# Kernel tuning notes

Hardware: AMD Instinct MI355X
Metric: run time of the kernel (lower is better)

Reference implementation:

```python
import jax, jax.numpy as jnp
import numpy as np


def setup_inputs() -> dict:
    key = jax.random.key(0)
    ks = jax.random.split(key, 6)
    B, S, D, G, I, H = 4, 2048, 1024, 256, 1024, 16
    return {
        "inputs_embeds": jax.random.normal(ks[0], (B, S, D), dtype=jnp.float32),
        "structure_features": jax.random.normal(ks[1], (B, G), dtype=jnp.float32),
        "Wq": jax.random.normal(ks[2], (D, I), dtype=jnp.float32) * 0.02,
        "Wk": jax.random.normal(ks[3], (G, I), dtype=jnp.float32) * 0.02,
        "Wv": jax.random.normal(ks[4], (D, I), dtype=jnp.float32) * 0.02,
        "Wo": jax.random.normal(ks[5], (I, D), dtype=jnp.float32) * 0.02,
        "num_heads": 16,
    }


def reference(inputs_embeds, structure_features, Wq, Wk, Wv, Wo, num_heads):
    B, S, D = inputs_embeds.shape
    I = Wq.shape[1]
    H = num_heads
    hd = I // H
    scale = 1.0 / (hd ** 0.5)

    # queries/values from token embeddings: [B, S, I] -> [B, H, S, hd]
    q = (inputs_embeds @ Wq).reshape(B, S, H, hd).transpose(0, 2, 1, 3)
    v = (inputs_embeds @ Wv).reshape(B, S, H, hd).transpose(0, 2, 1, 3)

    # structure_features is repeat-expanded to seq_len in the original; the
    # projection of identical rows is identical, so project once and broadcast.
    k1 = (structure_features @ Wk).reshape(B, 1, H, hd).transpose(0, 2, 1, 3)  # [B, H, 1, hd]
    k = jnp.broadcast_to(k1, (B, H, S, hd))  # same values as key_proj(repeated sf)

    # [B, H, S, S] score matrix (columns identical by construction, as in the
    # original module) -> softmax -> weighted sum of values.
    scores = jnp.einsum("bhqd,bhkd->bhqk", q, k) * scale
    probs = jax.nn.softmax(scores, axis=-1)
    attended = jnp.einsum("bhqk,bhkd->bhqd", probs, v)  # [B, H, S, hd]

    attended = attended.transpose(0, 2, 1, 3).reshape(B, S, I)
    return attended @ Wo
```

## Files before the change

### kernel.cpp

```cpp
#include <hip/hip_runtime.h>

#define BB 4
#define SS 2048
#define DD 1024
#define II 1024


constexpr int JP = 128;
constexpr int ROWS1 = SS / JP;

typedef float f4 __attribute__((ext_vector_type(4)));

__global__ __launch_bounds__(256)
void k1_partial(const float4* __restrict__ x, float4* __restrict__ pbuf) {
    const int g = blockIdx.x;
    const float4* xr = x + (size_t)g * ROWS1 * (DD / 4) + threadIdx.x;
    float4 a = make_float4(0.f, 0.f, 0.f, 0.f);
    #pragma unroll
    for (int r = 0; r < ROWS1; ++r) {
        float4 v = xr[(size_t)r * (DD / 4)];
        a.x += v.x; a.y += v.y; a.z += v.z; a.w += v.w;
    }
    pbuf[(size_t)g * (DD / 4) + threadIdx.x] = a;
}

__global__ __launch_bounds__(256)
void kred(const float4* __restrict__ pbuf, float4* __restrict__ xbar) {
    const int b = blockIdx.x >> 4, dg = blockIdx.x & 15;
    const int c4 = threadIdx.x & 15;
    const int jg = threadIdx.x >> 4;
    const float4* p = pbuf + ((size_t)b * JP + jg * 8) * (DD / 4) + dg * 16 + c4;
    float4 a = make_float4(0.f, 0.f, 0.f, 0.f);
    #pragma unroll
    for (int j = 0; j < 8; ++j) {
        float4 v = p[(size_t)j * (DD / 4)];
        a.x += v.x; a.y += v.y; a.z += v.z; a.w += v.w;
    }
    __shared__ float4 red[16][16];
    red[jg][c4] = a;
    __syncthreads();
    if (threadIdx.x < 16) {
        float4 s = make_float4(0.f, 0.f, 0.f, 0.f);
        #pragma unroll
        for (int q = 0; q < 16; ++q) {
            float4 v = red[q][threadIdx.x];
            s.x += v.x; s.y += v.y; s.z += v.z; s.w += v.w;
        }
        const float sc = 1.0f / (float)SS;
        xbar[b * (DD / 4) + dg * 16 + threadIdx.x] =
            make_float4(s.x * sc, s.y * sc, s.z * sc, s.w * sc);
    }
}

__global__ __launch_bounds__(1024)
void kg_gemv_b(const float4* __restrict__ vec, const float* __restrict__ W,
               float* __restrict__ out) {
    __shared__ float xs[DD];
    const int cg = blockIdx.x & 63;
    const int b  = blockIdx.x >> 6;
    const int tid = threadIdx.x;
    if (tid < DD / 4) ((f4*)xs)[tid] = ((const f4*)vec)[b * (DD / 4) + tid];
    __syncthreads();

    const int i0 = cg * 16;
    const int il = tid & 15, ks = tid >> 4;
    const float* wp = W + (size_t)(ks * 16) * DD + i0 + il;
    float a = 0.f;
    #pragma unroll
    for (int kk = 0; kk < 16; ++kk)
        a += xs[ks * 16 + kk] * wp[(size_t)kk * DD];

    __shared__ float red[64 * 16];
    __shared__ float red2[4 * 16];
    red[ks * 16 + il] = a;
    __syncthreads();
    if (tid < 64) {
        const int q = tid >> 4, i = tid & 15;
        float s = 0.f;
        #pragma unroll
        for (int k = 0; k < 16; ++k) s += red[(q * 16 + k) * 16 + i];
        red2[q * 16 + i] = s;
    }
    __syncthreads();
    if (tid < 16) {
        float s = red2[0 * 16 + tid] + red2[1 * 16 + tid]
                + red2[2 * 16 + tid] + red2[3 * 16 + tid];
        out[b * DD + i0 + tid] = s;
    }
}

__global__ __launch_bounds__(256)
void k4_bcast(const f4* __restrict__ orow, f4* __restrict__ out) {
    const int g = blockIdx.x;
    const int b = g >> 9;
    const int s0 = (g & 511) * 4;
    const f4 c = orow[b * (DD / 4) + threadIdx.x];
    f4* o = out + (size_t)(b * SS + s0) * (DD / 4) + threadIdx.x;
    #pragma unroll
    for (int r = 0; r < 4; ++r)
        __builtin_nontemporal_store(c, o + (size_t)r * (DD / 4));
}

extern "C" void kernel_launch(void* const* d_in, const int* in_sizes, int n_in,
                              void* d_out, int out_size, void* d_ws, size_t ws_size,
                              hipStream_t stream) {
    const float* x  = (const float*)d_in[0];
    const float* Wv = (const float*)d_in[4];
    const float* Wo = (const float*)d_in[5];
    float* out = (float*)d_out;

    float* pbuf = (float*)d_ws;
    float* xbar = pbuf + (size_t)BB * JP * DD;
    float* tvec = xbar + (size_t)BB * DD;
    float* orow = tvec + (size_t)BB * II;

    k1_partial<<<BB * JP, 256, 0, stream>>>((const float4*)x, (float4*)pbuf);
    kred<<<64, 256, 0, stream>>>((const float4*)pbuf, (float4*)xbar);
    kg_gemv_b<<<256, 1024, 0, stream>>>((const float4*)xbar, Wv, tvec);
    kg_gemv_b<<<256, 1024, 0, stream>>>((const float4*)tvec, Wo, orow);
    k4_bcast<<<(BB * SS) / 4, 256, 0, stream>>>((const f4*)orow, (f4*)out);
}
```

Baseline: 109.4 us.

## Fuse second GEMV with output broadcast and use nontemporal loads for input reduction

The second matrix-vector product is fused with the broadcast of the result row across all sequence positions, so one kernel launch and the orow round trip go away. The input column-sum kernel now uses nontemporal vector loads. The trade-off is in the fused kernel's stores: each block writes scalar floats to 16 contiguous columns, strided across rows. The old broadcast wrote full 16-byte vectors over contiguous rows, so write coalescing and width get worse, and only 256 blocks carry all the output traffic.

```diff
diff --git a/kernel.cpp b/kernel.cpp
--- a/kernel.cpp
+++ b/kernel.cpp
@@ -12,54 +12,46 @@
 typedef float f4 __attribute__((ext_vector_type(4)));
 
 __global__ __launch_bounds__(256)
-void k1_partial(const float4* __restrict__ x, float4* __restrict__ pbuf) {
+void k1_partial(const f4* __restrict__ x, f4* __restrict__ pbuf) {
     const int g = blockIdx.x;
-    const float4* xr = x + (size_t)g * ROWS1 * (DD / 4) + threadIdx.x;
-    float4 a = make_float4(0.f, 0.f, 0.f, 0.f);
+    const f4* xr = x + (size_t)g * ROWS1 * (DD / 4) + threadIdx.x;
+    f4 a = (f4)(0.f);
     #pragma unroll
-    for (int r = 0; r < ROWS1; ++r) {
-        float4 v = xr[(size_t)r * (DD / 4)];
-        a.x += v.x; a.y += v.y; a.z += v.z; a.w += v.w;
-    }
+    for (int r = 0; r < ROWS1; ++r)
+        a += __builtin_nontemporal_load(xr + (size_t)r * (DD / 4));
     pbuf[(size_t)g * (DD / 4) + threadIdx.x] = a;
 }
 
 __global__ __launch_bounds__(256)
-void kred(const float4* __restrict__ pbuf, float4* __restrict__ xbar) {
+void kred(const f4* __restrict__ pbuf, f4* __restrict__ xbar) {
     const int b = blockIdx.x >> 4, dg = blockIdx.x & 15;
     const int c4 = threadIdx.x & 15;
     const int jg = threadIdx.x >> 4;
-    const float4* p = pbuf + ((size_t)b * JP + jg * 8) * (DD / 4) + dg * 16 + c4;
-    float4 a = make_float4(0.f, 0.f, 0.f, 0.f);
+    const f4* p = pbuf + ((size_t)b * JP + jg * 8) * (DD / 4) + dg * 16 + c4;
+    f4 a = (f4)(0.f);
     #pragma unroll
-    for (int j = 0; j < 8; ++j) {
-        float4 v = p[(size_t)j * (DD / 4)];
-        a.x += v.x; a.y += v.y; a.z += v.z; a.w += v.w;
-    }
-    __shared__ float4 red[16][16];
+    for (int j = 0; j < 8; ++j)
+        a += p[(size_t)j * (DD / 4)];
+    __shared__ f4 red[16][16];
     red[jg][c4] = a;
     __syncthreads();
     if (threadIdx.x < 16) {
-        float4 s = make_float4(0.f, 0.f, 0.f, 0.f);
+        f4 s = (f4)(0.f);
         #pragma unroll
-        for (int q = 0; q < 16; ++q) {
-            float4 v = red[q][threadIdx.x];
-            s.x += v.x; s.y += v.y; s.z += v.z; s.w += v.w;
-        }
-        const float sc = 1.0f / (float)SS;
-        xbar[b * (DD / 4) + dg * 16 + threadIdx.x] =
-            make_float4(s.x * sc, s.y * sc, s.z * sc, s.w * sc);
+        for (int q = 0; q < 16; ++q)
+            s += red[q][threadIdx.x];
+        xbar[b * (DD / 4) + dg * 16 + threadIdx.x] = s * (1.0f / (float)SS);
     }
 }
 
 __global__ __launch_bounds__(1024)
-void kg_gemv_b(const float4* __restrict__ vec, const float* __restrict__ W,
+void kg_gemv_b(const f4* __restrict__ vec, const float* __restrict__ W,
                float* __restrict__ out) {
     __shared__ float xs[DD];
     const int cg = blockIdx.x & 63;
     const int b  = blockIdx.x >> 6;
     const int tid = threadIdx.x;
-    if (tid < DD / 4) ((f4*)xs)[tid] = ((const f4*)vec)[b * (DD / 4) + tid];
+    if (tid < DD / 4) ((f4*)xs)[tid] = vec[b * (DD / 4) + tid];
     __syncthreads();
 
     const int i0 = cg * 16;
@@ -89,16 +81,48 @@
     }
 }
 
-__global__ __launch_bounds__(256)
-void k4_bcast(const f4* __restrict__ orow, f4* __restrict__ out) {
-    const int g = blockIdx.x;
-    const int b = g >> 9;
-    const int s0 = (g & 511) * 4;
-    const f4 c = orow[b * (DD / 4) + threadIdx.x];
-    f4* o = out + (size_t)(b * SS + s0) * (DD / 4) + threadIdx.x;
+__global__ __launch_bounds__(1024)
+void kg2_bcast(const f4* __restrict__ vec, const float* __restrict__ W,
+               float* __restrict__ out) {
+    __shared__ float xs[DD];
+    const int cg = blockIdx.x & 63;
+    const int b  = blockIdx.x >> 6;
+    const int tid = threadIdx.x;
+    if (tid < DD / 4) ((f4*)xs)[tid] = vec[b * (DD / 4) + tid];
+    __syncthreads();
+
+    const int i0 = cg * 16;
+    const int il = tid & 15, ks = tid >> 4;
+    const float* wp = W + (size_t)(ks * 16) * DD + i0 + il;
+    float a = 0.f;
     #pragma unroll
-    for (int r = 0; r < 4; ++r)
-        __builtin_nontemporal_store(c, o + (size_t)r * (DD / 4));
+    for (int kk = 0; kk < 16; ++kk)
+        a += xs[ks * 16 + kk] * wp[(size_t)kk * DD];
+
+    __shared__ float red[64 * 16];
+    __shared__ float red2[4 * 16];
+    __shared__ float orow16[16];
+    red[ks * 16 + il] = a;
+    __syncthreads();
+    if (tid < 64) {
+        const int q = tid >> 4, i = tid & 15;
+        float s = 0.f;
+        #pragma unroll
+        for (int k = 0; k < 16; ++k) s += red[(q * 16 + k) * 16 + i];
+        red2[q * 16 + i] = s;
+    }
+    __syncthreads();
+    if (tid < 16)
+        orow16[tid] = red2[0 * 16 + tid] + red2[1 * 16 + tid]
+                    + red2[2 * 16 + tid] + red2[3 * 16 + tid];
+    __syncthreads();
+
+    const float c = orow16[il];
+    const int sg = tid >> 4;
+    float* o = out + (size_t)b * SS * DD + (size_t)sg * DD + i0 + il;
+    #pragma unroll
+    for (int r = 0; r < SS / 64; ++r)
+        __builtin_nontemporal_store(c, o + (size_t)r * 64 * DD);
 }
 
 extern "C" void kernel_launch(void* const* d_in, const int* in_sizes, int n_in,
@@ -112,11 +136,9 @@
     float* pbuf = (float*)d_ws;
     float* xbar = pbuf + (size_t)BB * JP * DD;
     float* tvec = xbar + (size_t)BB * DD;
-    float* orow = tvec + (size_t)BB * II;
 
-    k1_partial<<<BB * JP, 256, 0, stream>>>((const float4*)x, (float4*)pbuf);
-    kred<<<64, 256, 0, stream>>>((const float4*)pbuf, (float4*)xbar);
-    kg_gemv_b<<<256, 1024, 0, stream>>>((const float4*)xbar, Wv, tvec);
-    kg_gemv_b<<<256, 1024, 0, stream>>>((const float4*)tvec, Wo, orow);
-    k4_bcast<<<(BB * SS) / 4, 256, 0, stream>>>((const f4*)orow, (f4*)out);
+    k1_partial<<<BB * JP, 256, 0, stream>>>((const f4*)x, (f4*)pbuf);
+    kred<<<64, 256, 0, stream>>>((const f4*)pbuf, (f4*)xbar);
+    kg_gemv_b<<<256, 1024, 0, stream>>>((const f4*)xbar, Wv, tvec);
+    kg2_bcast<<<256, 1024, 0, stream>>>((const f4*)tvec, Wo, out);
 }
```

After: 110.5 us. No clear change (+1.0%).
